# Kernel optimization log

Hardware: AMD Instinct MI355X
Metric: run time of the kernel (lower is better)

## Reference

```python
import jax, jax.numpy as jnp
import numpy as np

HEADS, LEVELS, POINTS, DIMS = 8, 4, 4, 256
CH = DIMS // HEADS
SHAPES = np.array([[96, 96], [48, 48], [24, 24], [12, 12]], dtype=np.int64)
LEVEL_START = np.concatenate([[0], np.cumsum(SHAPES[:, 0] * SHAPES[:, 1])[:-1]]).astype(np.int64)
HW = int((SHAPES[:, 0] * SHAPES[:, 1]).sum())
N, Q = 2, HW


def setup_inputs() -> dict:
    key = jax.random.key(0)
    ks = jax.random.split(key, 8)
    return {
        "q": jax.random.normal(ks[0], (N, Q, DIMS), jnp.float32),
        "p": jax.random.uniform(ks[1], (N, Q, LEVELS, 2), jnp.float32),
        "v": jax.random.normal(ks[2], (N, HW, DIMS), jnp.float32),
        "W_off": jax.random.normal(ks[3], (DIMS, HEADS * LEVELS * POINTS * 2), jnp.float32) * 0.01,
        "b_off": jax.random.normal(ks[4], (HEADS * LEVELS * POINTS * 2,), jnp.float32) * 0.5,
        "W_attn": jax.random.normal(ks[5], (DIMS, HEADS * LEVELS * POINTS), jnp.float32) * 0.02,
        "b_attn": jnp.zeros((HEADS * LEVELS * POINTS,), jnp.float32),
        "W_in": jax.random.normal(ks[6], (DIMS, DIMS), jnp.float32) / np.float32(np.sqrt(DIMS)),
        "b_in": jnp.zeros((DIMS,), jnp.float32),
        "W_out": jax.random.normal(ks[7], (DIMS, DIMS), jnp.float32) / np.float32(np.sqrt(DIMS)),
        "b_out": jnp.zeros((DIMS,), jnp.float32),
        "shapes": jnp.asarray(SHAPES),
        "level_index": jnp.asarray(LEVEL_START),
    }


def _sample_level(vl, loc_l, Hl, Wl):
    """Bilinear sample with zero padding outside the feature map.
    vl: [N, Hl*Wl, heads, C]; loc_l: [N, Q, heads, P, 2] normalized (x, y) in [0,1].
    Returns [N, Q, P, heads, C]."""
    Nb, Qn, Hd, P, _ = loc_l.shape
    x = loc_l[..., 0] * Wl - 0.5  # pixel coords, align_corners=False convention
    y = loc_l[..., 1] * Hl - 0.5
    x0 = jnp.floor(x)
    y0 = jnp.floor(y)
    dx = x - x0
    dy = y - y0
    x0i = x0.astype(jnp.int32)
    y0i = y0.astype(jnp.int32)
    out = jnp.zeros((Nb, Qn, P, Hd, vl.shape[-1]), vl.dtype)
    corners = ((x0i, y0i, (1 - dx) * (1 - dy)), (x0i + 1, y0i, dx * (1 - dy)),
               (x0i, y0i + 1, (1 - dx) * dy), (x0i + 1, y0i + 1, dx * dy))
    for cx, cy, w in corners:
        valid = (cx >= 0) & (cx < Wl) & (cy >= 0) & (cy < Hl)
        idx = jnp.clip(cy, 0, Hl - 1) * Wl + jnp.clip(cx, 0, Wl - 1)  # [N,Q,Hd,P]
        idx_t = idx.transpose(0, 1, 3, 2).reshape(Nb, Qn * P, Hd, 1)
        g = jnp.take_along_axis(vl, idx_t, axis=1).reshape(Nb, Qn, P, Hd, -1)
        wv = jnp.where(valid, w, 0.0).transpose(0, 1, 3, 2)  # [N,Q,P,Hd]
        out = out + g * wv[..., None].astype(vl.dtype)
    return out


def _forward(q, p, v, W_off, b_off, W_attn, b_attn, W_in, b_in, W_out, b_out, shp, lsi):
    Nb, Qn, _ = q.shape
    v = (v @ W_in + b_in).reshape(Nb, -1, HEADS, CH)
    off = (q @ W_off + b_off).reshape(Nb, Qn, HEADS, LEVELS, POINTS, 2)
    attn = jax.nn.softmax((q @ W_attn + b_attn).reshape(Nb, Qn, HEADS, LEVELS * POINTS), axis=-1)
    attn = attn.reshape(Nb, Qn, HEADS, LEVELS, POINTS)
    # offsets normalized by (W, H) of each level, added to reference points (2-coord branch)
    off_norm = jnp.asarray(np.stack([shp[:, 1], shp[:, 0]], -1), q.dtype)  # [L, 2]
    loc = p[:, :, None, :, None, :] + off / off_norm[None, None, None, :, None, :]  # [N,Q,Hd,L,P,2]
    out = jnp.zeros((Nb, Qn, HEADS, CH), q.dtype)
    for l in range(LEVELS):
        Hl, Wl = int(shp[l, 0]), int(shp[l, 1])
        s = int(lsi[l])
        vl = jax.lax.slice_in_dim(v, s, s + Hl * Wl, axis=1)
        samp = _sample_level(vl, loc[:, :, :, l], Hl, Wl)  # [N,Q,P,Hd,C]
        out = out + jnp.einsum('nqphc,nqhp->nqhc', samp, attn[:, :, :, l])
    return out.reshape(Nb, Qn, DIMS) @ W_out + b_out


def reference(q, p, v, W_off, b_off, W_attn, b_attn, W_in, b_in, W_out, b_out, shapes, level_index):
    shp = np.asarray(shapes)  # spatial shapes are structural constants
    lsi = np.asarray(level_index)
    return _forward(q, p, v, W_off, b_off, W_attn, b_attn, W_in, b_in, W_out, b_out, shp, lsi)
```

## Files before the change

kernel.cpp:

```cpp
#include <hip/hip_runtime.h>
#include <hip/hip_bf16.h>
#include <math.h>

#define NB      2
#define QN      12240
#define HW_TOT  12240
#define DIMS    256
#define HEADS   8
#define CH      32
#define LEVELS  4
#define POINTS  4
#define M_TOT   (NB * QN)

typedef unsigned short ushort_t;
typedef __attribute__((ext_vector_type(8))) short short8;
typedef __attribute__((ext_vector_type(4))) float floatx4;

__device__ __constant__ int c_Hl[4]    = {96, 48, 24, 12};
__device__ __constant__ int c_Wl[4]    = {96, 48, 24, 12};
__device__ __constant__ int c_start[4] = {0, 9216, 11520, 12096};

__device__ __forceinline__ ushort_t f2bf(float f) {
    __hip_bfloat16 h = __float2bfloat16(f);
    return *reinterpret_cast<ushort_t*>(&h);
}

__global__ __launch_bounds__(256) void convert_qv_kernel(
    const float* __restrict__ v, const float* __restrict__ q,
    ushort_t* __restrict__ vbf, ushort_t* __restrict__ qbf)
{
    const size_t i = ((size_t)blockIdx.x * 256 + threadIdx.x) * 8;
    const size_t half = (size_t)M_TOT * DIMS;
    const float* src; ushort_t* dst; size_t off;
    if (i < half) { src = v; dst = vbf; off = i; }
    else          { src = q; dst = qbf; off = i - half; }
    const float4 a = *(const float4*)&src[off];
    const float4 b = *(const float4*)&src[off + 4];
    ushort_t t[8] = {f2bf(a.x), f2bf(a.y), f2bf(a.z), f2bf(a.w),
                     f2bf(b.x), f2bf(b.y), f2bf(b.z), f2bf(b.w)};
    *(int4*)&dst[off] = *(int4*)t;
}

__global__ __launch_bounds__(256) void prep_weights_kernel(
    const float* __restrict__ W_in, const float* __restrict__ W_off,
    const float* __restrict__ W_attn, const float* __restrict__ W_out,
    const float* __restrict__ b_off, const float* __restrict__ b_attn,
    ushort_t* __restrict__ Tin, ushort_t* __restrict__ Tcomb,
    ushort_t* __restrict__ Tout, float* __restrict__ bcomb)
{
    const int z  = blockIdx.z;
    const int gi = blockIdx.x * 256 + threadIdx.x;
    if (z == 1 && gi < 384)
        bcomb[gi] = (gi < 256) ? b_off[gi] : b_attn[gi - 256];
    const int Nw = (z == 1) ? 384 : 256;
    if (gi >= Nw * 256) return;
    const int k = gi & 255;
    const int n = gi >> 8;
    float val; ushort_t* T;
    if (z == 0)      { val = W_in[k * 256 + n];  T = Tin;  }
    else if (z == 1) { val = (n < 256) ? W_off[k * 256 + n]
                                       : W_attn[k * 128 + (n - 256)]; T = Tcomb; }
    else             { val = W_out[k * 256 + n]; T = Tout; }
    T[n * 256 + k] = f2bf(val);
}

__device__ __forceinline__ void storeval(float* C, size_t i, float v)    { C[i] = v; }
__device__ __forceinline__ void storeval(ushort_t* C, size_t i, float v) { C[i] = f2bf(v); }

template<typename OutT>
__global__ __launch_bounds__(256) void gemm_bf16_kernel(
    const ushort_t* __restrict__ A, const ushort_t* __restrict__ BT,
    const float* __restrict__ bias, OutT* __restrict__ C,
    int M, int Nc, int K)
{
    __shared__ ushort_t As[128 * 32];
    __shared__ ushort_t Bs[64 * 32];

    const int tid  = threadIdx.x;
    const int wave = tid >> 6;
    const int lane = tid & 63;
    const int quad = lane >> 4;
    const int l16  = lane & 15;
    const int wm   = (wave >> 1) * 64;
    const int wn   = (wave & 1) * 32;
    const int bm0  = blockIdx.x * 128;
    const int bn0  = blockIdx.y * 64;

    const int arow = tid >> 2;
    const int akc  = (tid & 3) * 8;

    floatx4 acc[4][2];
    #pragma unroll
    for (int i = 0; i < 4; ++i)
        #pragma unroll
        for (int j = 0; j < 2; ++j)
            acc[i][j] = (floatx4){0.f, 0.f, 0.f, 0.f};

    int ga0 = bm0 + arow;      if (ga0 > M - 1) ga0 = M - 1;
    int ga1 = bm0 + arow + 64; if (ga1 > M - 1) ga1 = M - 1;

    for (int kk = 0; kk < K; kk += 32) {
        const int4 va0 = *(const int4*)&A[(size_t)ga0 * K + kk + akc];
        const int4 va1 = *(const int4*)&A[(size_t)ga1 * K + kk + akc];
        const int4 vb  = *(const int4*)&BT[(size_t)(bn0 + arow) * K + kk + akc];
        *(int4*)&As[arow * 32 + akc]        = va0;
        *(int4*)&As[(arow + 64) * 32 + akc] = va1;
        *(int4*)&Bs[arow * 32 + akc]        = vb;
        __syncthreads();

        short8 af[4], bfr[2];
        #pragma unroll
        for (int mt = 0; mt < 4; ++mt)
            af[mt] = *(const short8*)&As[(wm + mt * 16 + l16) * 32 + quad * 8];
        #pragma unroll
        for (int nt = 0; nt < 2; ++nt)
            bfr[nt] = *(const short8*)&Bs[(wn + nt * 16 + l16) * 32 + quad * 8];
        #pragma unroll
        for (int mt = 0; mt < 4; ++mt)
            #pragma unroll
            for (int nt = 0; nt < 2; ++nt)
                acc[mt][nt] = __builtin_amdgcn_mfma_f32_16x16x32_bf16(
                    af[mt], bfr[nt], acc[mt][nt], 0, 0, 0);
        __syncthreads();
    }

    #pragma unroll
    for (int mt = 0; mt < 4; ++mt) {
        #pragma unroll
        for (int j = 0; j < 4; ++j) {
            const int row = bm0 + wm + mt * 16 + quad * 4 + j;
            if (row >= M) continue;
            #pragma unroll
            for (int nt = 0; nt < 2; ++nt) {
                const int col = bn0 + wn + nt * 16 + l16;
                storeval(C, (size_t)row * Nc + col, acc[mt][nt][j] + bias[col]);
            }
        }
    }
}

#define QB 4
#define SLOTS 576

__global__ __launch_bounds__(256) void msda_sample_kernel(
    const ushort_t* __restrict__ vproj, const float* __restrict__ offlog,
    const float* __restrict__ p, ushort_t* __restrict__ mid)
{
    __shared__ float s_logit[QB][128];
    __shared__ float s_off[QB][256];
    __shared__ float s_p[QB][8];
    __shared__ float s_mx[QB][HEADS];
    __shared__ float s_inv[QB][HEADS];
    __shared__ float s_w[QB][SLOTS];
    __shared__ int   s_idx[QB][SLOTS];

    const int tid = threadIdx.x;
    const int bq0 = blockIdx.x * QB;

    #pragma unroll
    for (int i = tid; i < QB * 256; i += 256) {
        int sub = i >> 8, j = i & 255;
        s_off[sub][j] = offlog[(size_t)(bq0 + sub) * 384 + j];
    }
    #pragma unroll
    for (int i = tid; i < QB * 128; i += 256) {
        int sub = i >> 7, j = i & 127;
        s_logit[sub][j] = offlog[(size_t)(bq0 + sub) * 384 + 256 + j];
    }
    if (tid < QB * 8) {
        int sub = tid >> 3, j = tid & 7;
        s_p[sub][j] = p[(size_t)(bq0 + sub) * 8 + j];
    }
    __syncthreads();

    if (tid < QB * HEADS) {
        int sub = tid >> 3, h = tid & 7;
        float mx = -1e30f;
        #pragma unroll
        for (int i = 0; i < 16; ++i) mx = fmaxf(mx, s_logit[sub][h * 16 + i]);
        float ssum = 0.0f;
        #pragma unroll
        for (int i = 0; i < 16; ++i) ssum += __expf(s_logit[sub][h * 16 + i] - mx);
        s_mx[sub][h] = mx;
        s_inv[sub][h] = 1.0f / ssum;
    }
    __syncthreads();

    #pragma unroll
    for (int tt = tid; tt < QB * 128; tt += 256) {
        const int sub = tt >> 7;
        const int j   = tt & 127;
        const int h   = j >> 4;
        const int l   = (j >> 2) & 3;
        const int nq  = bq0 + sub;
        const int nb  = (nq >= QN) ? 1 : 0;

        const int Hl = c_Hl[l], Wl = c_Wl[l], st = c_start[l];
        const float fW = (float)Wl, fH = (float)Hl;

        const float w = __expf(s_logit[sub][j] - s_mx[sub][h]) * s_inv[sub][h];

        const int oi = j * 2;
        const float ox = s_off[sub][oi];
        const float oy = s_off[sub][oi + 1];
        const float px = s_p[sub][l * 2 + 0];
        const float py = s_p[sub][l * 2 + 1];

        const float lx = px + ox / fW;
        const float ly = py + oy / fH;
        const float x = lx * fW - 0.5f;
        const float y = ly * fH - 0.5f;

        const float x0f = floorf(x), y0f = floorf(y);
        const int x0 = (int)x0f, y0 = (int)y0f;
        const float dx = x - x0f, dy = y - y0f;

        const int base = nb * (HW_TOT * DIMS) + h * CH;
        const int slot = (j & 15) * 36 + h * 4;

        const bool vx0 = (x0 >= 0) & (x0 < Wl);
        const bool vx1 = (x0 + 1 >= 0) & (x0 + 1 < Wl);
        const bool vy0 = (y0 >= 0) & (y0 < Hl);
        const bool vy1 = (y0 + 1 >= 0) & (y0 + 1 < Hl);

        s_w[sub][slot + 0] = (vx0 & vy0) ? w * (1.0f - dx) * (1.0f - dy) : 0.0f;
        s_w[sub][slot + 1] = (vx1 & vy0) ? w * dx * (1.0f - dy) : 0.0f;
        s_w[sub][slot + 2] = (vx0 & vy1) ? w * (1.0f - dx) * dy : 0.0f;
        s_w[sub][slot + 3] = (vx1 & vy1) ? w * dx * dy : 0.0f;
        s_idx[sub][slot + 0] = (vx0 & vy0) ? base + (st + y0 * Wl + x0) * DIMS : 0;
        s_idx[sub][slot + 1] = (vx1 & vy0) ? base + (st + y0 * Wl + x0 + 1) * DIMS : 0;
        s_idx[sub][slot + 2] = (vx0 & vy1) ? base + (st + (y0 + 1) * Wl + x0) * DIMS : 0;
        s_idx[sub][slot + 3] = (vx1 & vy1) ? base + (st + (y0 + 1) * Wl + x0 + 1) * DIMS : 0;
    }
    __syncthreads();

    const int sub  = tid >> 6;
    const int lane = tid & 63;
    const int h    = lane >> 3;
    const int c4   = lane & 7;
    const int nq   = bq0 + sub;

    float ax = 0.0f, ay = 0.0f, az = 0.0f, aw = 0.0f;
    const ushort_t* __restrict__ vb = vproj + c4 * 4;

    #pragma unroll
    for (int t = 0; t < 16; ++t) {
        const int slot = t * 36 + h * 4;
        const int4   I = *(const int4*)&s_idx[sub][slot];
        const float4 W = *(const float4*)&s_w[sub][slot];

        const uint2 g0 = *(const uint2*)(vb + I.x);
        const uint2 g1 = *(const uint2*)(vb + I.y);
        const uint2 g2 = *(const uint2*)(vb + I.z);
        const uint2 g3 = *(const uint2*)(vb + I.w);

        ax = fmaf(W.x, __uint_as_float(g0.x << 16), ax);
        ay = fmaf(W.x, __uint_as_float(g0.x & 0xffff0000u), ay);
        az = fmaf(W.x, __uint_as_float(g0.y << 16), az);
        aw = fmaf(W.x, __uint_as_float(g0.y & 0xffff0000u), aw);

        ax = fmaf(W.y, __uint_as_float(g1.x << 16), ax);
        ay = fmaf(W.y, __uint_as_float(g1.x & 0xffff0000u), ay);
        az = fmaf(W.y, __uint_as_float(g1.y << 16), az);
        aw = fmaf(W.y, __uint_as_float(g1.y & 0xffff0000u), aw);

        ax = fmaf(W.z, __uint_as_float(g2.x << 16), ax);
        ay = fmaf(W.z, __uint_as_float(g2.x & 0xffff0000u), ay);
        az = fmaf(W.z, __uint_as_float(g2.y << 16), az);
        aw = fmaf(W.z, __uint_as_float(g2.y & 0xffff0000u), aw);

        ax = fmaf(W.w, __uint_as_float(g3.x << 16), ax);
        ay = fmaf(W.w, __uint_as_float(g3.x & 0xffff0000u), ay);
        az = fmaf(W.w, __uint_as_float(g3.y << 16), az);
        aw = fmaf(W.w, __uint_as_float(g3.y & 0xffff0000u), aw);
    }

    ushort_t mv[4] = {f2bf(ax), f2bf(ay), f2bf(az), f2bf(aw)};
    *(uint2*)&mid[(size_t)nq * DIMS + lane * 4] = *(uint2*)mv;
}

extern "C" void kernel_launch(void* const* d_in, const int* in_sizes, int n_in,
                              void* d_out, int out_size, void* d_ws, size_t ws_size,
                              hipStream_t stream)
{
    const float* q      = (const float*)d_in[0];
    const float* p      = (const float*)d_in[1];
    const float* v      = (const float*)d_in[2];
    const float* W_off  = (const float*)d_in[3];
    const float* b_off  = (const float*)d_in[4];
    const float* W_attn = (const float*)d_in[5];
    const float* b_attn = (const float*)d_in[6];
    const float* W_in   = (const float*)d_in[7];
    const float* b_in   = (const float*)d_in[8];
    const float* W_out  = (const float*)d_in[9];
    const float* b_out  = (const float*)d_in[10];
    float* out = (float*)d_out;

    const int M = M_TOT;

    ushort_t* vproj  = (ushort_t*)d_ws;
    float*    offlog = (float*)(vproj + (size_t)M * 256);
    ushort_t* vbf    = (ushort_t*)(offlog + (size_t)M * 384);
    ushort_t* mid    = vbf;
    ushort_t* qbf    = vbf + (size_t)M * 256;
    ushort_t* Tin    = qbf + (size_t)M * 256;
    ushort_t* Tcomb  = Tin + 256 * 256;
    ushort_t* Tout   = Tcomb + 384 * 256;
    float*    bcomb  = (float*)(Tout + 256 * 256);

    convert_qv_kernel<<<dim3(6120), 256, 0, stream>>>(v, q, vbf, qbf);
    prep_weights_kernel<<<dim3(384, 1, 3), 256, 0, stream>>>(
        W_in, W_off, W_attn, W_out, b_off, b_attn, Tin, Tcomb, Tout, bcomb);

    gemm_bf16_kernel<ushort_t><<<dim3(192, 4), 256, 0, stream>>>(
        vbf, Tin, b_in, vproj, M, 256, 256);
    gemm_bf16_kernel<float><<<dim3(192, 6), 256, 0, stream>>>(
        qbf, Tcomb, bcomb, offlog, M, 384, 256);
    msda_sample_kernel<<<dim3(M / QB), 256, 0, stream>>>(vproj, offlog, p, mid);
    gemm_bf16_kernel<float><<<dim3(192, 4), 256, 0, stream>>>(
        mid, Tout, b_out, out, M, 256, 256);
}
```

Before: 218.5 us.

## Widen GEMM tiles, use direct global-to-LDS loads, merge projection GEMMs, shrink sampler blocks

```diff
diff --git a/kernel.cpp b/kernel.cpp
--- a/kernel.cpp
+++ b/kernel.cpp
@@ -64,61 +64,70 @@
     T[n * 256 + k] = f2bf(val);
 }
 
-__device__ __forceinline__ void storeval(float* C, size_t i, float v)    { C[i] = v; }
-__device__ __forceinline__ void storeval(ushort_t* C, size_t i, float v) { C[i] = f2bf(v); }
-
-template<typename OutT>
-__global__ __launch_bounds__(256) void gemm_bf16_kernel(
+__device__ __forceinline__ void gemm_tile_core(
     const ushort_t* __restrict__ A, const ushort_t* __restrict__ BT,
-    const float* __restrict__ bias, OutT* __restrict__ C,
-    int M, int Nc, int K)
-{
-    __shared__ ushort_t As[128 * 32];
-    __shared__ ushort_t Bs[64 * 32];
-
+    const float* __restrict__ bias, void* __restrict__ C, bool c_bf16,
+    int M, int Nc, int bm0, int bn0, int K,
+    ushort_t* As, ushort_t* Bs)
+{
     const int tid  = threadIdx.x;
     const int wave = tid >> 6;
     const int lane = tid & 63;
     const int quad = lane >> 4;
     const int l16  = lane & 15;
     const int wm   = (wave >> 1) * 64;
-    const int wn   = (wave & 1) * 32;
-    const int bm0  = blockIdx.x * 128;
-    const int bn0  = blockIdx.y * 64;
-
-    const int arow = tid >> 2;
-    const int akc  = (tid & 3) * 8;
-
-    floatx4 acc[4][2];
+    const int wn   = (wave & 1) * 64;
+
+    const int off0 = tid * 16;
+    const int row0 = off0 >> 6;
+    const int kc0  = (off0 & 63) >> 1;
+
+    int ar0 = bm0 + row0;      if (ar0 > M - 1) ar0 = M - 1;
+    int ar1 = bm0 + row0 + 64; if (ar1 > M - 1) ar1 = M - 1;
+
+    const ushort_t* ga0 = A  + (size_t)ar0 * K + kc0;
+    const ushort_t* ga1 = A  + (size_t)ar1 * K + kc0;
+    const ushort_t* gb0 = BT + (size_t)(bn0 + row0) * K + kc0;
+    const ushort_t* gb1 = BT + (size_t)(bn0 + row0 + 64) * K + kc0;
+
+    ushort_t* lA0 = As + wave * 512;
+    ushort_t* lA1 = As + wave * 512 + 2048;
+    ushort_t* lB0 = Bs + wave * 512;
+    ushort_t* lB1 = Bs + wave * 512 + 2048;
+
+    floatx4 acc[4][4];
     #pragma unroll
     for (int i = 0; i < 4; ++i)
         #pragma unroll
-        for (int j = 0; j < 2; ++j)
+        for (int j = 0; j < 4; ++j)
             acc[i][j] = (floatx4){0.f, 0.f, 0.f, 0.f};
 
-    int ga0 = bm0 + arow;      if (ga0 > M - 1) ga0 = M - 1;
-    int ga1 = bm0 + arow + 64; if (ga1 > M - 1) ga1 = M - 1;
-
     for (int kk = 0; kk < K; kk += 32) {
-        const int4 va0 = *(const int4*)&A[(size_t)ga0 * K + kk + akc];
-        const int4 va1 = *(const int4*)&A[(size_t)ga1 * K + kk + akc];
-        const int4 vb  = *(const int4*)&BT[(size_t)(bn0 + arow) * K + kk + akc];
-        *(int4*)&As[arow * 32 + akc]        = va0;
-        *(int4*)&As[(arow + 64) * 32 + akc] = va1;
-        *(int4*)&Bs[arow * 32 + akc]        = vb;
+        __builtin_amdgcn_global_load_lds(
+            (const __attribute__((address_space(1))) void*)(ga0 + kk),
+            (__attribute__((address_space(3))) void*)lA0, 16, 0, 0);
+        __builtin_amdgcn_global_load_lds(
+            (const __attribute__((address_space(1))) void*)(ga1 + kk),
+            (__attribute__((address_space(3))) void*)lA1, 16, 0, 0);
+        __builtin_amdgcn_global_load_lds(
+            (const __attribute__((address_space(1))) void*)(gb0 + kk),
+            (__attribute__((address_space(3))) void*)lB0, 16, 0, 0);
+        __builtin_amdgcn_global_load_lds(
+            (const __attribute__((address_space(1))) void*)(gb1 + kk),
+            (__attribute__((address_space(3))) void*)lB1, 16, 0, 0);
         __syncthreads();
 
-        short8 af[4], bfr[2];
+        short8 af[4], bfr[4];
         #pragma unroll
         for (int mt = 0; mt < 4; ++mt)
             af[mt] = *(const short8*)&As[(wm + mt * 16 + l16) * 32 + quad * 8];
         #pragma unroll
-        for (int nt = 0; nt < 2; ++nt)
+        for (int nt = 0; nt < 4; ++nt)
             bfr[nt] = *(const short8*)&Bs[(wn + nt * 16 + l16) * 32 + quad * 8];
         #pragma unroll
         for (int mt = 0; mt < 4; ++mt)
             #pragma unroll
-            for (int nt = 0; nt < 2; ++nt)
+            for (int nt = 0; nt < 4; ++nt)
                 acc[mt][nt] = __builtin_amdgcn_mfma_f32_16x16x32_bf16(
                     af[mt], bfr[nt], acc[mt][nt], 0, 0, 0);
         __syncthreads();
@@ -131,18 +140,46 @@
             const int row = bm0 + wm + mt * 16 + quad * 4 + j;
             if (row >= M) continue;
             #pragma unroll
-            for (int nt = 0; nt < 2; ++nt) {
+            for (int nt = 0; nt < 4; ++nt) {
                 const int col = bn0 + wn + nt * 16 + l16;
-                storeval(C, (size_t)row * Nc + col, acc[mt][nt][j] + bias[col]);
+                const float val = acc[mt][nt][j] + bias[col];
+                if (c_bf16) ((ushort_t*)C)[(size_t)row * Nc + col] = f2bf(val);
+                else        ((float*)C)[(size_t)row * Nc + col]    = val;
             }
         }
     }
 }
 
-#define QB 4
+__global__ __launch_bounds__(256) void gemm_proj_kernel(
+    const ushort_t* __restrict__ vbf, const ushort_t* __restrict__ qbf,
+    const ushort_t* __restrict__ Tin, const ushort_t* __restrict__ Tcomb,
+    const float* __restrict__ b_in, const float* __restrict__ bcomb,
+    ushort_t* __restrict__ vproj, float* __restrict__ offlog)
+{
+    __shared__ ushort_t As[128 * 32];
+    __shared__ ushort_t Bs[128 * 32];
+    const int bm0 = blockIdx.x * 128;
+    const int y = blockIdx.y;
+    if (y < 2)
+        gemm_tile_core(vbf, Tin, b_in, vproj, true, M_TOT, 256, bm0, y * 128, 256, As, Bs);
+    else
+        gemm_tile_core(qbf, Tcomb, bcomb, offlog, false, M_TOT, 384, bm0, (y - 2) * 128, 256, As, Bs);
+}
+
+__global__ __launch_bounds__(256) void gemm_out_kernel(
+    const ushort_t* __restrict__ mid, const ushort_t* __restrict__ Tout,
+    const float* __restrict__ b_out, float* __restrict__ out)
+{
+    __shared__ ushort_t As[128 * 32];
+    __shared__ ushort_t Bs[128 * 32];
+    gemm_tile_core(mid, Tout, b_out, out, false, M_TOT, 256,
+                   blockIdx.x * 128, blockIdx.y * 128, 256, As, Bs);
+}
+
+#define QB 2
 #define SLOTS 576
 
-__global__ __launch_bounds__(256) void msda_sample_kernel(
+__global__ __launch_bounds__(128) void msda_sample_kernel(
     const ushort_t* __restrict__ vproj, const float* __restrict__ offlog,
     const float* __restrict__ p, ushort_t* __restrict__ mid)
 {
@@ -158,12 +195,12 @@
     const int bq0 = blockIdx.x * QB;
 
     #pragma unroll
-    for (int i = tid; i < QB * 256; i += 256) {
+    for (int i = tid; i < QB * 256; i += 128) {
         int sub = i >> 8, j = i & 255;
         s_off[sub][j] = offlog[(size_t)(bq0 + sub) * 384 + j];
     }
     #pragma unroll
-    for (int i = tid; i < QB * 128; i += 256) {
+    for (int i = tid; i < QB * 128; i += 128) {
         int sub = i >> 7, j = i & 127;
         s_logit[sub][j] = offlog[(size_t)(bq0 + sub) * 384 + 256 + j];
     }
@@ -187,7 +224,7 @@
     __syncthreads();
 
     #pragma unroll
-    for (int tt = tid; tt < QB * 128; tt += 256) {
+    for (int tt = tid; tt < QB * 128; tt += 128) {
         const int sub = tt >> 7;
         const int j   = tt & 127;
         const int h   = j >> 4;
@@ -312,11 +349,8 @@
     prep_weights_kernel<<<dim3(384, 1, 3), 256, 0, stream>>>(
         W_in, W_off, W_attn, W_out, b_off, b_attn, Tin, Tcomb, Tout, bcomb);
 
-    gemm_bf16_kernel<ushort_t><<<dim3(192, 4), 256, 0, stream>>>(
-        vbf, Tin, b_in, vproj, M, 256, 256);
-    gemm_bf16_kernel<float><<<dim3(192, 6), 256, 0, stream>>>(
-        qbf, Tcomb, bcomb, offlog, M, 384, 256);
-    msda_sample_kernel<<<dim3(M / QB), 256, 0, stream>>>(vproj, offlog, p, mid);
-    gemm_bf16_kernel<float><<<dim3(192, 4), 256, 0, stream>>>(
-        mid, Tout, b_out, out, M, 256, 256);
-}
+    gemm_proj_kernel<<<dim3(192, 5), 256, 0, stream>>>(
+        vbf, qbf, Tin, Tcomb, b_in, bcomb, vproj, offlog);
+    msda_sample_kernel<<<dim3(M / QB), 128, 0, stream>>>(vproj, offlog, p, mid);
+    gemm_out_kernel<<<dim3(192, 2), 256, 0, stream>>>(mid, Tout, b_out, out);
+}
```

After: 208.6 us. 4.5% less time.
